# Optimization experiments

Measured on AMD Instinct MI355X. Metric: run time of the kernel, lower is better.

## Reference

```python
import jax, jax.numpy as jnp
import numpy as np

N_NODES = 100000
N_EDGES = 3200000
F_IN = 512
HIDDEN = 16
N_CLASSES = 16


def setup_inputs() -> dict:
    key = jax.random.key(0)
    k1, k2, k3, k4 = jax.random.split(key, 4)
    x = jax.random.normal(k1, (N_NODES, F_IN), dtype=jnp.float32)
    edge_index = jax.random.randint(k2, (2, N_EDGES), 0, N_NODES, dtype=jnp.int32)
    # Glorot-style init for GCN weights
    W1 = jax.random.normal(k3, (F_IN, HIDDEN), dtype=jnp.float32) * np.float32(np.sqrt(2.0 / (F_IN + HIDDEN)))
    b1 = jnp.zeros((HIDDEN,), dtype=jnp.float32)
    W2 = jax.random.normal(k4, (HIDDEN, N_CLASSES), dtype=jnp.float32) * np.float32(np.sqrt(2.0 / (HIDDEN + N_CLASSES)))
    b2 = jnp.zeros((N_CLASSES,), dtype=jnp.float32)
    return {"x": x, "W1": W1, "b1": b1, "W2": W2, "b2": b2, "edge_index": edge_index}


def _gcn_conv(x, src, dst, W, b, n_nodes):
    """PyG GCNConv: h = x @ W, then symmetric-normalized aggregation with self-loops, + bias."""
    h = x @ W  # [N, out]
    # degrees include self-loops (edge weight 1.0 everywhere)
    ones = jnp.ones(src.shape[0], dtype=h.dtype)
    deg = jax.ops.segment_sum(ones, dst, num_segments=n_nodes) + 1.0  # +1 for self-loop
    dinv = jax.lax.rsqrt(deg)  # deg >= 1, no zero guard needed
    norm = dinv[src] * dinv[dst]  # [E]
    agg = jax.ops.segment_sum(h[src] * norm[:, None], dst, num_segments=n_nodes)
    # self-loop contribution: norm_ii = 1/deg_i
    agg = agg + h * (dinv * dinv)[:, None]
    return agg + b


def reference(x, W1, b1, W2, b2, edge_index):
    src, dst = edge_index[0], edge_index[1]
    n = x.shape[0]
    h = jax.nn.relu(_gcn_conv(x, src, dst, W1, b1, n))
    # dropout is identity in eval mode
    out = _gcn_conv(h, src, dst, W2, b2, n)
    return jax.nn.log_softmax(out, axis=1)
```

## Files before the change

kernel.cpp:

```cpp
#include <hip/hip_runtime.h>
#include <hip/hip_bf16.h>
#include <math.h>

constexpr int N_NODES = 100000;
constexpr int N_EDGES = 3200000;
constexpr int F_IN    = 512;
constexpr int HID     = 16;

constexpr int NPAD = 100352;

constexpr int B_BITS = 8;
constexpr int NPB    = 1 << B_BITS;
constexpr int NBKT   = (N_NODES + NPB - 1) / NPB;
constexpr int SBLK   = 400;
constexpr int CHUNK  = N_EDGES / SBLK;
constexpr int MAX_BKT_E = 12288;

typedef float f32x4 __attribute__((ext_vector_type(4)));
typedef short bfrag8 __attribute__((ext_vector_type(8)));

__device__ __forceinline__ unsigned short f2bf_rne(float f) {
    unsigned int u = __float_as_uint(f);
    u += 0x7FFFu + ((u >> 16) & 1u);
    return (unsigned short)(u >> 16);
}

__global__ __launch_bounds__(1024) void bin_count_kernel(const int* __restrict__ dst,
                                                         int* __restrict__ gcnt) {
    __shared__ int cnt[NBKT];
    const int tid = threadIdx.x;
    for (int t = tid; t < NBKT; t += 1024) cnt[t] = 0;
    __syncthreads();
    const int base = blockIdx.x * CHUNK;
    for (int i = tid; i < CHUNK; i += 1024)
        atomicAdd(&cnt[dst[base + i] >> B_BITS], 1);
    __syncthreads();
    for (int t = tid; t < NBKT; t += 1024)
        if (cnt[t]) atomicAdd(&gcnt[t], cnt[t]);
}

__global__ __launch_bounds__(512) void bucket_scan_kernel(const int* __restrict__ gcnt,
                                                          int* __restrict__ bbase,
                                                          int* __restrict__ gcur) {
    __shared__ int s[512];
    const int tid = threadIdx.x;
    s[tid] = (tid < NBKT) ? gcnt[tid] : 0;
    __syncthreads();
    for (int off = 1; off < 512; off <<= 1) {
        int v = (tid >= off) ? s[tid - off] : 0;
        __syncthreads();
        s[tid] += v;
        __syncthreads();
    }
    int excl = (tid == 0) ? 0 : s[tid - 1];
    if (tid <= NBKT) bbase[tid] = excl;
    if (tid <  NBKT) gcur[tid]  = excl;
}

__global__ __launch_bounds__(1024) void bin_scatter_kernel(const int* __restrict__ src,
                                                           const int* __restrict__ dst,
                                                           int* __restrict__ gcur,
                                                           unsigned int* __restrict__ binned) {
    __shared__ int cnt[NBKT];
    __shared__ int cur[NBKT];
    const int tid = threadIdx.x;
    for (int t = tid; t < NBKT; t += 1024) cnt[t] = 0;
    __syncthreads();
    const int base = blockIdx.x * CHUNK;
    for (int i = tid; i < CHUNK; i += 1024)
        atomicAdd(&cnt[dst[base + i] >> B_BITS], 1);
    __syncthreads();
    for (int t = tid; t < NBKT; t += 1024)
        cur[t] = cnt[t] ? atomicAdd(&gcur[t], cnt[t]) : 0;
    __syncthreads();
    for (int i = tid; i < CHUNK; i += 1024) {
        int d = dst[base + i];
        int b = d >> B_BITS;
        int pos = atomicAdd(&cur[b], 1);
        binned[pos] = ((unsigned)(d & (NPB - 1)) << 24) | (unsigned)src[base + i];
    }
}

__global__ __launch_bounds__(1024) void csr_bucket_kernel(const unsigned int* __restrict__ binned,
                                                          const int* __restrict__ bbase,
                                                          int* __restrict__ row,
                                                          int* __restrict__ csr,
                                                          float* __restrict__ dinv) {
    __shared__ unsigned int eb[MAX_BKT_E];
    __shared__ int deg[NPB];
    __shared__ int pre[NPB];
    __shared__ int cur[NPB];
    const int tid = threadIdx.x;
    const int b = blockIdx.x;
    const int e0 = bbase[b];
    int ne = bbase[b + 1] - e0;
    if (ne > MAX_BKT_E) ne = MAX_BKT_E;

    if (tid < NPB) deg[tid] = 0;
    for (int i = tid; i < ne; i += 1024) eb[i] = binned[e0 + i];
    __syncthreads();
    for (int i = tid; i < ne; i += 1024)
        atomicAdd(&deg[eb[i] >> 24], 1);
    __syncthreads();
    if (tid < NPB) pre[tid] = deg[tid];
    __syncthreads();
    for (int off = 1; off < NPB; off <<= 1) {
        int v = 0;
        if (tid < NPB && tid >= off) v = pre[tid - off];
        __syncthreads();
        if (tid < NPB) pre[tid] += v;
        __syncthreads();
    }
    if (tid < NPB) {
        int excl = (tid == 0) ? 0 : pre[tid - 1];
        int g = e0 + excl;
        cur[tid] = g;
        int node = b * NPB + tid;
        if (node < N_NODES) {
            row[node] = g;
            dinv[node] = rsqrtf((float)deg[tid] + 1.0f);
        }
    }
    if (b == 0 && tid == 0) row[N_NODES] = N_EDGES;
    __syncthreads();
    for (int i = tid; i < ne; i += 1024) {
        unsigned int v = eb[i];
        int pos = atomicAdd(&cur[v >> 24], 1);
        csr[pos] = (int)(v & 0xFFFFFFu);
    }
}

__global__ __launch_bounds__(256) void w1prep_kernel(const float* __restrict__ W1,
                                                     unsigned short* __restrict__ w1t) {
    int i = blockIdx.x * 256 + threadIdx.x;
    if (i < F_IN * HID) {
        int k = i >> 4, n = i & 15;
        w1t[n * F_IN + k] = f2bf_rne(W1[i]);
    }
}

__global__ __launch_bounds__(256) void gemm1_kernel(const float* __restrict__ x,
                                                    const unsigned short* __restrict__ w1t,
                                                    const float* __restrict__ b1,
                                                    const float* __restrict__ dinv,
                                                    float* __restrict__ hh,
                                                    float* __restrict__ agg1) {
    __shared__ unsigned short xs[64 * 520];
    const int tid = threadIdx.x;
    const int node0 = blockIdx.x * 64;

    #pragma unroll
    for (int r = 0; r < 32; ++r) {
        int idx = (r * 256 + tid) * 4;
        int ln = idx >> 9;
        int k  = idx & 511;
        int gn = node0 + ln; if (gn >= N_NODES) gn = N_NODES - 1;
        float4 v = *(const float4*)(x + (size_t)gn * F_IN + k);
        ushort4 bv;
        bv.x = f2bf_rne(v.x); bv.y = f2bf_rne(v.y);
        bv.z = f2bf_rne(v.z); bv.w = f2bf_rne(v.w);
        *(ushort4*)(xs + ln * 520 + k) = bv;
    }

    const int lane = tid & 63;
    const int wv   = tid >> 6;
    const int m    = lane & 15;
    const int quad = lane >> 4;

    bfrag8 bfr[16];
    const unsigned short* wbase = w1t + m * F_IN + quad * 8;
    #pragma unroll
    for (int t = 0; t < 16; ++t)
        bfr[t] = *(const bfrag8*)(wbase + t * 32);

    __syncthreads();

    f32x4 acc = {0.f, 0.f, 0.f, 0.f};
    const unsigned short* arow = xs + (wv * 16 + m) * 520 + quad * 8;
    #pragma unroll
    for (int t = 0; t < 16; ++t) {
        bfrag8 afr = *(const bfrag8*)(arow + t * 32);
        acc = __builtin_amdgcn_mfma_f32_16x16x32_bf16(afr, bfr[t], acc, 0, 0, 0);
    }

    const float b1j = b1[m];
    #pragma unroll
    for (int r = 0; r < 4; ++r) {
        int gn = node0 + wv * 16 + quad * 4 + r;
        if (gn < N_NODES) {
            float dv = dinv[gn];
            float hv = acc[r] * dv;
            size_t o = (size_t)gn * 16 + m;
            hh[o] = hv;
            agg1[o] = hv * dv + b1j;
        }
    }
}

__global__ __launch_bounds__(256) void pull_kernel(const float* __restrict__ hh,
                                                   const float* __restrict__ dinv,
                                                   const int* __restrict__ row,
                                                   const int* __restrict__ csr,
                                                   float* __restrict__ agg) {
    int t = blockIdx.x * 256 + threadIdx.x;
    int node = t >> 4;
    int j = t & 15;
    if (node >= N_NODES) return;
    int p = row[node], end = row[node + 1];
    float a0 = 0.f, a1 = 0.f, a2 = 0.f, a3 = 0.f;
    for (; p + 4 <= end; p += 4) {
        int s0 = csr[p], s1 = csr[p + 1], s2 = csr[p + 2], s3 = csr[p + 3];
        a0 += hh[(s0 << 4) + j];
        a1 += hh[(s1 << 4) + j];
        a2 += hh[(s2 << 4) + j];
        a3 += hh[(s3 << 4) + j];
    }
    for (; p < end; ++p) a0 += hh[(csr[p] << 4) + j];
    float acc = (a0 + a1) + (a2 + a3);
    agg[(node << 4) + j] += dinv[node] * acc;
}

__global__ __launch_bounds__(256) void layer2_kernel(const float* __restrict__ agg1,
                                                     const float* __restrict__ W2,
                                                     const float* __restrict__ b2,
                                                     const float* __restrict__ dinv,
                                                     float* __restrict__ hh2,
                                                     float* __restrict__ agg2) {
    __shared__ float w2s[256];
    __shared__ float b2s[16];
    const int tid = threadIdx.x;
    w2s[tid] = W2[tid];
    if (tid < 16) b2s[tid] = b2[tid];
    __syncthreads();
    int i = blockIdx.x * 256 + tid;
    if (i >= N_NODES) return;
    float v[16];
    const float4* ar = (const float4*)(agg1 + (size_t)i * 16);
    float4 r0 = ar[0], r1 = ar[1], r2 = ar[2], r3 = ar[3];
    v[0]=r0.x; v[1]=r0.y; v[2]=r0.z; v[3]=r0.w;
    v[4]=r1.x; v[5]=r1.y; v[6]=r1.z; v[7]=r1.w;
    v[8]=r2.x; v[9]=r2.y; v[10]=r2.z; v[11]=r2.w;
    v[12]=r3.x; v[13]=r3.y; v[14]=r3.z; v[15]=r3.w;
    #pragma unroll
    for (int k = 0; k < 16; ++k) v[k] = fmaxf(v[k], 0.f);
    float dv = dinv[i], dv2 = dv * dv;
    float o[16];
    #pragma unroll
    for (int jj = 0; jj < 16; ++jj) {
        float s = 0.f;
        #pragma unroll
        for (int k = 0; k < 16; ++k) s += v[k] * w2s[k * 16 + jj];
        o[jj] = s;
    }
    float4* ho = (float4*)(hh2 + (size_t)i * 16);
    float4* ao = (float4*)(agg2 + (size_t)i * 16);
    ho[0] = make_float4(o[0]*dv,  o[1]*dv,  o[2]*dv,  o[3]*dv);
    ho[1] = make_float4(o[4]*dv,  o[5]*dv,  o[6]*dv,  o[7]*dv);
    ho[2] = make_float4(o[8]*dv,  o[9]*dv,  o[10]*dv, o[11]*dv);
    ho[3] = make_float4(o[12]*dv, o[13]*dv, o[14]*dv, o[15]*dv);
    ao[0] = make_float4(o[0]*dv2+b2s[0],  o[1]*dv2+b2s[1],  o[2]*dv2+b2s[2],  o[3]*dv2+b2s[3]);
    ao[1] = make_float4(o[4]*dv2+b2s[4],  o[5]*dv2+b2s[5],  o[6]*dv2+b2s[6],  o[7]*dv2+b2s[7]);
    ao[2] = make_float4(o[8]*dv2+b2s[8],  o[9]*dv2+b2s[9],  o[10]*dv2+b2s[10],o[11]*dv2+b2s[11]);
    ao[3] = make_float4(o[12]*dv2+b2s[12],o[13]*dv2+b2s[13],o[14]*dv2+b2s[14],o[15]*dv2+b2s[15]);
}

__global__ __launch_bounds__(256) void lsm_kernel(const float* __restrict__ agg2,
                                                  float* __restrict__ out) {
    int i = blockIdx.x * 256 + threadIdx.x;
    if (i >= N_NODES) return;
    float v[16];
    const float4* ar = (const float4*)(agg2 + (size_t)i * 16);
    float4 r0 = ar[0], r1 = ar[1], r2 = ar[2], r3 = ar[3];
    v[0]=r0.x; v[1]=r0.y; v[2]=r0.z; v[3]=r0.w;
    v[4]=r1.x; v[5]=r1.y; v[6]=r1.z; v[7]=r1.w;
    v[8]=r2.x; v[9]=r2.y; v[10]=r2.z; v[11]=r2.w;
    v[12]=r3.x; v[13]=r3.y; v[14]=r3.z; v[15]=r3.w;
    float m = v[0];
    #pragma unroll
    for (int k = 1; k < 16; ++k) m = fmaxf(m, v[k]);
    float ssum = 0.f;
    #pragma unroll
    for (int k = 0; k < 16; ++k) ssum += expf(v[k] - m);
    float l = m + logf(ssum);
    float4* oo = (float4*)(out + (size_t)i * 16);
    oo[0] = make_float4(v[0]-l, v[1]-l, v[2]-l, v[3]-l);
    oo[1] = make_float4(v[4]-l, v[5]-l, v[6]-l, v[7]-l);
    oo[2] = make_float4(v[8]-l, v[9]-l, v[10]-l, v[11]-l);
    oo[3] = make_float4(v[12]-l, v[13]-l, v[14]-l, v[15]-l);
}

extern "C" void kernel_launch(void* const* d_in, const int* in_sizes, int n_in,
                              void* d_out, int out_size, void* d_ws, size_t ws_size,
                              hipStream_t stream) {
    const float* x    = (const float*)d_in[0];
    const float* W1   = (const float*)d_in[1];
    const float* b1   = (const float*)d_in[2];
    const float* W2   = (const float*)d_in[3];
    const float* b2   = (const float*)d_in[4];
    const int*   ei   = (const int*)d_in[5];
    const int*   src  = ei;
    const int*   dst  = ei + N_EDGES;
    float* out = (float*)d_out;

    int*   wsi  = (int*)d_ws;
    float* wsf  = (float*)d_ws;
    int*   gcnt  = wsi;
    int*   bbase = wsi + 512;
    int*   gcur  = wsi + 1024;
    float* dinv  = wsf + 2048;
    int*   row   = wsi + 2048 + NPAD;
    int*   csr   = wsi + 2048 + 2 * NPAD;
    unsigned int* binned = (unsigned int*)csr;
    float* hh    = wsf + 2048 + 2 * NPAD + N_EDGES;
    float* agg1  = hh   + (size_t)N_NODES * 16;
    float* hh2   = agg1 + (size_t)N_NODES * 16;
    float* agg2  = hh2  + (size_t)N_NODES * 16;
    unsigned short* w1t = (unsigned short*)(agg2 + (size_t)N_NODES * 16);

    const int NB = (N_NODES + 255) / 256;
    const int GB = N_NODES / 16;
    const int MB = (N_NODES + 63) / 64;

    hipMemsetAsync(gcnt, 0, NBKT * sizeof(int), stream);
    bin_count_kernel <<<SBLK, 1024, 0, stream>>>(dst, gcnt);
    bucket_scan_kernel<<<1, 512, 0, stream>>>(gcnt, bbase, gcur);
    bin_scatter_kernel<<<SBLK, 1024, 0, stream>>>(src, dst, gcur, binned);
    csr_bucket_kernel<<<NBKT, 1024, 0, stream>>>(binned, bbase, row, csr, dinv);
    w1prep_kernel<<<32, 256, 0, stream>>>(W1, w1t);
    gemm1_kernel<<<MB, 256, 0, stream>>>(x, w1t, b1, dinv, hh, agg1);
    pull_kernel<<<GB, 256, 0, stream>>>(hh, dinv, row, csr, agg1);
    layer2_kernel<<<NB, 256, 0, stream>>>(agg1, W2, b2, dinv, hh2, agg2);
    pull_kernel<<<GB, 256, 0, stream>>>(hh2, dinv, row, csr, agg2);
    lsm_kernel<<<NB, 256, 0, stream>>>(agg2, out);
}
```

Before: 493.0 us.

## Fuse layer2 and log_softmax into pulls, store gathered features as bf16, drop LDS staging

The layer-2 dense transform (relu, W2 matmul via shuffles) is folded into the first aggregation kernel, and log_softmax into the second, which removes two launches and their round trips through intermediate buffers. The per-node features read by the gathers are stored as bf16, halving the bytes of the random gather traffic. gemm1 now loads x directly from global memory into registers and converts to bf16 per MFMA fragment instead of staging through shared memory. Using bf16 for the gathered messages adds rounding error, and the uncoalesced direct loads in gemm1 may change its bandwidth efficiency.

```diff
diff --git a/kernel.cpp b/kernel.cpp
--- a/kernel.cpp
+++ b/kernel.cpp
@@ -23,6 +23,9 @@
     unsigned int u = __float_as_uint(f);
     u += 0x7FFFu + ((u >> 16) & 1u);
     return (unsigned short)(u >> 16);
+}
+__device__ __forceinline__ float bf2f(unsigned short u) {
+    return __uint_as_float((unsigned int)u << 16);
 }
 
 __global__ __launch_bounds__(1024) void bin_count_kernel(const int* __restrict__ dst,
@@ -143,29 +146,17 @@
                                                     const unsigned short* __restrict__ w1t,
                                                     const float* __restrict__ b1,
                                                     const float* __restrict__ dinv,
-                                                    float* __restrict__ hh,
-                                                    float* __restrict__ agg1) {
-    __shared__ unsigned short xs[64 * 520];
-    const int tid = threadIdx.x;
-    const int node0 = blockIdx.x * 64;
-
-    #pragma unroll
-    for (int r = 0; r < 32; ++r) {
-        int idx = (r * 256 + tid) * 4;
-        int ln = idx >> 9;
-        int k  = idx & 511;
-        int gn = node0 + ln; if (gn >= N_NODES) gn = N_NODES - 1;
-        float4 v = *(const float4*)(x + (size_t)gn * F_IN + k);
-        ushort4 bv;
-        bv.x = f2bf_rne(v.x); bv.y = f2bf_rne(v.y);
-        bv.z = f2bf_rne(v.z); bv.w = f2bf_rne(v.w);
-        *(ushort4*)(xs + ln * 520 + k) = bv;
-    }
-
+                                                    unsigned short* __restrict__ hh_bf,
+                                                    float* __restrict__ aggs1) {
+    const int tid  = threadIdx.x;
     const int lane = tid & 63;
     const int wv   = tid >> 6;
     const int m    = lane & 15;
     const int quad = lane >> 4;
+    const int node0 = blockIdx.x * 64 + wv * 16;
+
+    int gm = node0 + m; if (gm >= N_NODES) gm = N_NODES - 1;
+    const float* arow = x + (size_t)gm * F_IN + quad * 8;
 
     bfrag8 bfr[16];
     const unsigned short* wbase = w1t + m * F_IN + quad * 8;
@@ -173,120 +164,111 @@
     for (int t = 0; t < 16; ++t)
         bfr[t] = *(const bfrag8*)(wbase + t * 32);
 
-    __syncthreads();
-
     f32x4 acc = {0.f, 0.f, 0.f, 0.f};
-    const unsigned short* arow = xs + (wv * 16 + m) * 520 + quad * 8;
-    #pragma unroll
+    #pragma unroll 4
     for (int t = 0; t < 16; ++t) {
-        bfrag8 afr = *(const bfrag8*)(arow + t * 32);
+        float4 lo = *(const float4*)(arow + t * 32);
+        float4 hi = *(const float4*)(arow + t * 32 + 4);
+        bfrag8 afr;
+        afr[0] = (short)f2bf_rne(lo.x); afr[1] = (short)f2bf_rne(lo.y);
+        afr[2] = (short)f2bf_rne(lo.z); afr[3] = (short)f2bf_rne(lo.w);
+        afr[4] = (short)f2bf_rne(hi.x); afr[5] = (short)f2bf_rne(hi.y);
+        afr[6] = (short)f2bf_rne(hi.z); afr[7] = (short)f2bf_rne(hi.w);
         acc = __builtin_amdgcn_mfma_f32_16x16x32_bf16(afr, bfr[t], acc, 0, 0, 0);
     }
 
     const float b1j = b1[m];
     #pragma unroll
     for (int r = 0; r < 4; ++r) {
-        int gn = node0 + wv * 16 + quad * 4 + r;
+        int gn = node0 + quad * 4 + r;
         if (gn < N_NODES) {
             float dv = dinv[gn];
             float hv = acc[r] * dv;
             size_t o = (size_t)gn * 16 + m;
-            hh[o] = hv;
-            agg1[o] = hv * dv + b1j;
+            hh_bf[o] = f2bf_rne(hv);
+            aggs1[o] = hv * dv + b1j;
         }
     }
 }
 
-__global__ __launch_bounds__(256) void pull_kernel(const float* __restrict__ hh,
-                                                   const float* __restrict__ dinv,
-                                                   const int* __restrict__ row,
-                                                   const int* __restrict__ csr,
-                                                   float* __restrict__ agg) {
-    int t = blockIdx.x * 256 + threadIdx.x;
+__global__ __launch_bounds__(256) void pull1_kernel(const unsigned short* __restrict__ hh_bf,
+                                                    const float* __restrict__ aggs1,
+                                                    const float* __restrict__ dinv,
+                                                    const int* __restrict__ row,
+                                                    const int* __restrict__ csr,
+                                                    const float* __restrict__ W2,
+                                                    const float* __restrict__ b2,
+                                                    unsigned short* __restrict__ hh2_bf,
+                                                    float* __restrict__ aggs2) {
+    __shared__ float w2s[256];
+    __shared__ float b2s[16];
+    const int tid = threadIdx.x;
+    w2s[tid] = W2[tid];
+    if (tid < 16) b2s[tid] = b2[tid];
+    __syncthreads();
+
+    int t = blockIdx.x * 256 + tid;
     int node = t >> 4;
     int j = t & 15;
-    if (node >= N_NODES) return;
     int p = row[node], end = row[node + 1];
     float a0 = 0.f, a1 = 0.f, a2 = 0.f, a3 = 0.f;
     for (; p + 4 <= end; p += 4) {
         int s0 = csr[p], s1 = csr[p + 1], s2 = csr[p + 2], s3 = csr[p + 3];
-        a0 += hh[(s0 << 4) + j];
-        a1 += hh[(s1 << 4) + j];
-        a2 += hh[(s2 << 4) + j];
-        a3 += hh[(s3 << 4) + j];
-    }
-    for (; p < end; ++p) a0 += hh[(csr[p] << 4) + j];
-    float acc = (a0 + a1) + (a2 + a3);
-    agg[(node << 4) + j] += dinv[node] * acc;
-}
-
-__global__ __launch_bounds__(256) void layer2_kernel(const float* __restrict__ agg1,
-                                                     const float* __restrict__ W2,
-                                                     const float* __restrict__ b2,
-                                                     const float* __restrict__ dinv,
-                                                     float* __restrict__ hh2,
-                                                     float* __restrict__ agg2) {
-    __shared__ float w2s[256];
-    __shared__ float b2s[16];
-    const int tid = threadIdx.x;
-    w2s[tid] = W2[tid];
-    if (tid < 16) b2s[tid] = b2[tid];
-    __syncthreads();
-    int i = blockIdx.x * 256 + tid;
-    if (i >= N_NODES) return;
-    float v[16];
-    const float4* ar = (const float4*)(agg1 + (size_t)i * 16);
-    float4 r0 = ar[0], r1 = ar[1], r2 = ar[2], r3 = ar[3];
-    v[0]=r0.x; v[1]=r0.y; v[2]=r0.z; v[3]=r0.w;
-    v[4]=r1.x; v[5]=r1.y; v[6]=r1.z; v[7]=r1.w;
-    v[8]=r2.x; v[9]=r2.y; v[10]=r2.z; v[11]=r2.w;
-    v[12]=r3.x; v[13]=r3.y; v[14]=r3.z; v[15]=r3.w;
+        a0 += bf2f(hh_bf[(s0 << 4) + j]);
+        a1 += bf2f(hh_bf[(s1 << 4) + j]);
+        a2 += bf2f(hh_bf[(s2 << 4) + j]);
+        a3 += bf2f(hh_bf[(s3 << 4) + j]);
+    }
+    for (; p < end; ++p) a0 += bf2f(hh_bf[(csr[p] << 4) + j]);
+    float dv = dinv[node];
+    float aj = aggs1[(node << 4) + j] + dv * ((a0 + a1) + (a2 + a3));
+    float vj = fmaxf(aj, 0.f);
+
+    float h2 = 0.f;
     #pragma unroll
-    for (int k = 0; k < 16; ++k) v[k] = fmaxf(v[k], 0.f);
-    float dv = dinv[i], dv2 = dv * dv;
-    float o[16];
-    #pragma unroll
-    for (int jj = 0; jj < 16; ++jj) {
-        float s = 0.f;
-        #pragma unroll
-        for (int k = 0; k < 16; ++k) s += v[k] * w2s[k * 16 + jj];
-        o[jj] = s;
-    }
-    float4* ho = (float4*)(hh2 + (size_t)i * 16);
-    float4* ao = (float4*)(agg2 + (size_t)i * 16);
-    ho[0] = make_float4(o[0]*dv,  o[1]*dv,  o[2]*dv,  o[3]*dv);
-    ho[1] = make_float4(o[4]*dv,  o[5]*dv,  o[6]*dv,  o[7]*dv);
-    ho[2] = make_float4(o[8]*dv,  o[9]*dv,  o[10]*dv, o[11]*dv);
-    ho[3] = make_float4(o[12]*dv, o[13]*dv, o[14]*dv, o[15]*dv);
-    ao[0] = make_float4(o[0]*dv2+b2s[0],  o[1]*dv2+b2s[1],  o[2]*dv2+b2s[2],  o[3]*dv2+b2s[3]);
-    ao[1] = make_float4(o[4]*dv2+b2s[4],  o[5]*dv2+b2s[5],  o[6]*dv2+b2s[6],  o[7]*dv2+b2s[7]);
-    ao[2] = make_float4(o[8]*dv2+b2s[8],  o[9]*dv2+b2s[9],  o[10]*dv2+b2s[10],o[11]*dv2+b2s[11]);
-    ao[3] = make_float4(o[12]*dv2+b2s[12],o[13]*dv2+b2s[13],o[14]*dv2+b2s[14],o[15]*dv2+b2s[15]);
-}
-
-__global__ __launch_bounds__(256) void lsm_kernel(const float* __restrict__ agg2,
-                                                  float* __restrict__ out) {
-    int i = blockIdx.x * 256 + threadIdx.x;
-    if (i >= N_NODES) return;
-    float v[16];
-    const float4* ar = (const float4*)(agg2 + (size_t)i * 16);
-    float4 r0 = ar[0], r1 = ar[1], r2 = ar[2], r3 = ar[3];
-    v[0]=r0.x; v[1]=r0.y; v[2]=r0.z; v[3]=r0.w;
-    v[4]=r1.x; v[5]=r1.y; v[6]=r1.z; v[7]=r1.w;
-    v[8]=r2.x; v[9]=r2.y; v[10]=r2.z; v[11]=r2.w;
-    v[12]=r3.x; v[13]=r3.y; v[14]=r3.z; v[15]=r3.w;
-    float m = v[0];
-    #pragma unroll
-    for (int k = 1; k < 16; ++k) m = fmaxf(m, v[k]);
-    float ssum = 0.f;
-    #pragma unroll
-    for (int k = 0; k < 16; ++k) ssum += expf(v[k] - m);
-    float l = m + logf(ssum);
-    float4* oo = (float4*)(out + (size_t)i * 16);
-    oo[0] = make_float4(v[0]-l, v[1]-l, v[2]-l, v[3]-l);
-    oo[1] = make_float4(v[4]-l, v[5]-l, v[6]-l, v[7]-l);
-    oo[2] = make_float4(v[8]-l, v[9]-l, v[10]-l, v[11]-l);
-    oo[3] = make_float4(v[12]-l, v[13]-l, v[14]-l, v[15]-l);
+    for (int k = 0; k < 16; ++k) {
+        float vk = __shfl(vj, k, 16);
+        h2 += vk * w2s[k * 16 + j];
+    }
+    size_t o = (size_t)node * 16 + j;
+    float hv = h2 * dv;
+    hh2_bf[o] = f2bf_rne(hv);
+    aggs2[o] = hv * dv + b2s[j];
+}
+
+__global__ __launch_bounds__(256) void pull2_kernel(const unsigned short* __restrict__ hh2_bf,
+                                                    const float* __restrict__ aggs2,
+                                                    const float* __restrict__ dinv,
+                                                    const int* __restrict__ row,
+                                                    const int* __restrict__ csr,
+                                                    float* __restrict__ out) {
+    int t = blockIdx.x * 256 + threadIdx.x;
+    int node = t >> 4;
+    int j = t & 15;
+    int p = row[node], end = row[node + 1];
+    float a0 = 0.f, a1 = 0.f, a2 = 0.f, a3 = 0.f;
+    for (; p + 4 <= end; p += 4) {
+        int s0 = csr[p], s1 = csr[p + 1], s2 = csr[p + 2], s3 = csr[p + 3];
+        a0 += bf2f(hh2_bf[(s0 << 4) + j]);
+        a1 += bf2f(hh2_bf[(s1 << 4) + j]);
+        a2 += bf2f(hh2_bf[(s2 << 4) + j]);
+        a3 += bf2f(hh2_bf[(s3 << 4) + j]);
+    }
+    for (; p < end; ++p) a0 += bf2f(hh2_bf[(csr[p] << 4) + j]);
+    float oj = aggs2[(node << 4) + j] + dinv[node] * ((a0 + a1) + (a2 + a3));
+
+    float mx = oj;
+    mx = fmaxf(mx, __shfl_xor(mx, 1));
+    mx = fmaxf(mx, __shfl_xor(mx, 2));
+    mx = fmaxf(mx, __shfl_xor(mx, 4));
+    mx = fmaxf(mx, __shfl_xor(mx, 8));
+    float e = expf(oj - mx);
+    float s = e;
+    s += __shfl_xor(s, 1);
+    s += __shfl_xor(s, 2);
+    s += __shfl_xor(s, 4);
+    s += __shfl_xor(s, 8);
+    out[(size_t)node * 16 + j] = oj - mx - logf(s);
 }
 
 extern "C" void kernel_launch(void* const* d_in, const int* in_sizes, int n_in,
@@ -311,13 +293,13 @@
     int*   row   = wsi + 2048 + NPAD;
     int*   csr   = wsi + 2048 + 2 * NPAD;
     unsigned int* binned = (unsigned int*)csr;
-    float* hh    = wsf + 2048 + 2 * NPAD + N_EDGES;
-    float* agg1  = hh   + (size_t)N_NODES * 16;
-    float* hh2   = agg1 + (size_t)N_NODES * 16;
-    float* agg2  = hh2  + (size_t)N_NODES * 16;
-    unsigned short* w1t = (unsigned short*)(agg2 + (size_t)N_NODES * 16);
-
-    const int NB = (N_NODES + 255) / 256;
+    const size_t off0 = 2048 + 2 * (size_t)NPAD + N_EDGES;
+    unsigned short* hh_bf  = (unsigned short*)(wsi + off0);
+    float*          aggs1  = wsf + off0 + 800000;
+    unsigned short* hh2_bf = (unsigned short*)(wsi + off0 + 2400000);
+    float*          aggs2  = wsf + off0 + 3200000;
+    unsigned short* w1t    = (unsigned short*)(wsi + off0 + 4800000);
+
     const int GB = N_NODES / 16;
     const int MB = (N_NODES + 63) / 64;
 
@@ -327,9 +309,7 @@
     bin_scatter_kernel<<<SBLK, 1024, 0, stream>>>(src, dst, gcur, binned);
     csr_bucket_kernel<<<NBKT, 1024, 0, stream>>>(binned, bbase, row, csr, dinv);
     w1prep_kernel<<<32, 256, 0, stream>>>(W1, w1t);
-    gemm1_kernel<<<MB, 256, 0, stream>>>(x, w1t, b1, dinv, hh, agg1);
-    pull_kernel<<<GB, 256, 0, stream>>>(hh, dinv, row, csr, agg1);
-    layer2_kernel<<<NB, 256, 0, stream>>>(agg1, W2, b2, dinv, hh2, agg2);
-    pull_kernel<<<GB, 256, 0, stream>>>(hh2, dinv, row, csr, agg2);
-    lsm_kernel<<<NB, 256, 0, stream>>>(agg2, out);
-}
+    gemm1_kernel<<<MB, 256, 0, stream>>>(x, w1t, b1, dinv, hh_bf, aggs1);
+    pull1_kernel<<<GB, 256, 0, stream>>>(hh_bf, aggs1, dinv, row, csr, W2, b2, hh2_bf, aggs2);
+    pull2_kernel<<<GB, 256, 0, stream>>>(hh2_bf, aggs2, dinv, row, csr, out);
+}
```

Result: faster. 483.0 us (-2.0%).
